# Optimization experiments

Measured on AMD Instinct MI355X. Metric: run time of the kernel, lower is better.

## Reference

```python
import jax, jax.numpy as jnp
from jax import lax
import numpy as np


def gen_position(p, pos_decay=1.0):
    # Fixed relative-position bias: (9, p*p), neighbor order di*3+dj
    ar = jnp.arange(p, dtype=jnp.float32)
    right = jnp.broadcast_to(jnp.exp(-ar / (p / pos_decay))[None, :], (p, p))  # decays along width
    down = right.T                                                             # decays along height
    i, j = jnp.meshgrid(ar, ar, indexing='ij')
    br = jnp.exp(-(i + j) / (p / pos_decay))
    ones = jnp.ones((p, p), jnp.float32)
    merge = jnp.stack([
        jnp.rot90(br, 2), down[::-1, :], jnp.rot90(br, 1),
        right[:, ::-1], ones, right,
        jnp.rot90(br, 3), down, br,
    ], axis=0)
    return merge.reshape(9, -1)


def attention_conv(x, w_qkv, b_qkv, head_w, window_size, num_heads):
    b, c, h, w = x.shape
    p = window_size // 3
    pad_h = (p * (1 + h // p) - h) % p
    pad_w = (p * (1 + w // p) - w) % p
    xp = jnp.pad(x, ((0, 0), (0, 0), (p + pad_h, p), (p + pad_w, p)), mode='reflect')
    Hp, Wp = xp.shape[2], xp.shape[3]
    nH, nW = Hp // p - 2, Wp // p - 2  # == number of unfold windows (stride p, size 3p)
    # Non-overlapping p x p tiles; each window = 3x3 grid of adjacent tiles.
    tiles = xp.reshape(b, c, nH + 2, p, nW + 2, p).transpose(0, 2, 4, 1, 3, 5)  # [b,nH+2,nW+2,c,p,p]
    neigh = jnp.stack([tiles[:, di:di + nH, dj:dj + nW]
                       for di in range(3) for dj in range(3)], axis=3)  # [b,nH,nW,9,c,p,p]
    L = c * p * p
    pp = p * p
    xw = neigh.reshape(b * nH * nW, 9, L)
    qkv = xw @ w_qkv.T + b_qkv                                  # [N,9,nh*3*L]
    qkv = qkv.reshape(-1, 9, num_heads, 3, c, pp).transpose(0, 2, 4, 3, 1, 5)  # [N,nh,C,3,9,pp]
    q, k, v = qkv[:, :, :, 0], qkv[:, :, :, 1], qkv[:, :, :, 2]  # each [N,nh,C,9,pp]
    bias = gen_position(p)                                       # [9,pp]
    core_q = q[:, :, :, 4, :]                                    # center patch query [N,nh,C,pp]
    score = jnp.einsum('nhcp,nhckp->nhck', core_q, k * bias) / jnp.sqrt(jnp.float32(L))
    attn = jax.nn.softmax(score, axis=-1)                        # over 9 neighbors
    out = jnp.einsum('nhck,nhckp->nhcp', attn, v).reshape(-1, num_heads, L)
    out = jnp.einsum('h,nhd->nd', head_w[0], out)                # head mixing [N,L]
    out = out.reshape(b, nH, nW, c, p, p).transpose(0, 3, 1, 4, 2, 5).reshape(b, c, nH * p, nW * p)
    return out[:, :, pad_h:, pad_w:]


def setup_inputs() -> dict:
    key = jax.random.key(0)
    ks = jax.random.split(key, 8)
    B, C, H, W = 4, 3, 256, 256
    x = jax.random.uniform(ks[0], (B, C, H, W), dtype=jnp.float32)
    # conv3: window 3, p=1, heads 6, L=3 ; conv6: window 6, p=2, heads 4, L=12 ; conv9: window 9, p=3, heads 2, L=27
    w3_qkv = jax.random.normal(ks[1], (6 * 3 * 3, 3), jnp.float32) * 0.2
    b3_qkv = jnp.zeros((6 * 3 * 3,), jnp.float32)
    hw3 = jnp.full((1, 6), 1.0 / 6.0, jnp.float32)
    w6_qkv = jax.random.normal(ks[2], (4 * 3 * 12, 12), jnp.float32) * 0.1
    b6_qkv = jnp.zeros((4 * 3 * 12,), jnp.float32)
    hw6 = jnp.full((1, 4), 1.0 / 4.0, jnp.float32)
    w9_qkv = jax.random.normal(ks[3], (2 * 3 * 27, 27), jnp.float32) * 0.07
    b9_qkv = jnp.zeros((2 * 3 * 27,), jnp.float32)
    hw9 = jnp.full((1, 2), 1.0 / 2.0, jnp.float32)
    conv0_w = jax.random.normal(ks[4], (3, 9, 5, 5), jnp.float32) * 0.05
    conv0_b = jnp.zeros((3,), jnp.float32)
    return {"x": x, "w3_qkv": w3_qkv, "b3_qkv": b3_qkv, "hw3": hw3,
            "w6_qkv": w6_qkv, "b6_qkv": b6_qkv, "hw6": hw6,
            "w9_qkv": w9_qkv, "b9_qkv": b9_qkv, "hw9": hw9,
            "conv0_w": conv0_w, "conv0_b": conv0_b}


def reference(x, w3_qkv, b3_qkv, hw3, w6_qkv, b6_qkv, hw6,
              w9_qkv, b9_qkv, hw9, conv0_w, conv0_b):
    b, c, h, w = x.shape
    # global prior: softmax over size-1 dim (== ones), then global max pool
    gavg = jnp.mean((1.0 - x).reshape(b, c, -1), axis=-1, keepdims=True)       # [b,c,1]
    x_g = jax.nn.softmax(gavg, axis=-1)[..., None]                             # [b,c,1,1]
    x_g = jnp.max((x * x_g).reshape(b, 1, -1), axis=-1, keepdims=True)[..., None]  # [b,1,1,1]
    x3 = attention_conv(x,  w3_qkv, b3_qkv, hw3, 3, 6)
    x6 = attention_conv(x3, w6_qkv, b6_qkv, hw6, 6, 4)
    x9 = attention_conv(x6, w9_qkv, b9_qkv, hw9, 9, 2)
    cat = jnp.concatenate([x9, x6, x3], axis=1)                                # [b,9,h,w]
    x0 = jax.nn.relu(lax.conv_general_dilated(cat, conv0_w, (1, 1), ((2, 2), (2, 2)),
                                              dimension_numbers=('NCHW', 'OIHW', 'NCHW'))
                     + conv0_b[None, :, None, None])
    return jax.nn.relu(x * x0 + (x_g - x0))
```

## Files before the change

kernel.cpp:

```cpp
#include <hip/hip_runtime.h>
#include <math.h>

__device__ __forceinline__ int refl256(int t) {
    t = t < 0 ? -t : t;
    return t > 255 ? 510 - t : t;
}

__global__ __launch_bounds__(256)
void attn_p1v(const float* __restrict__ x, const float* __restrict__ w,
              const float* __restrict__ bq, const float* __restrict__ hw,
              float* __restrict__ out, float* __restrict__ pmax)
{
    int t = blockIdx.x * 256 + threadIdx.x;
    int xx = t & 255, yp = (t >> 8) & 127, bb = t >> 15;
    int y0 = yp * 2;
    const float* xb = x + bb * 196608;
    int rs[4], cs[3];
#pragma unroll
    for (int dr = 0; dr < 4; ++dr) rs[dr] = refl256(y0 + dr - 1) << 8;
#pragma unroll
    for (int dc = 0; dc < 3; ++dc) cs[dc] = refl256(xx + dc - 1);
    float xw[4][3][3];
#pragma unroll
    for (int dr = 0; dr < 4; ++dr)
#pragma unroll
        for (int dc = 0; dc < 3; ++dc)
#pragma unroll
            for (int c = 0; c < 3; ++c)
                xw[dr][dc][c] = xb[c * 65536 + rs[dr] + cs[dc]];

    {
        float bm = 0.f;
#pragma unroll
        for (int c = 0; c < 3; ++c)
            bm = fmaxf(bm, fmaxf(xw[1][1][c], xw[2][1][c]));
#pragma unroll
        for (int off = 32; off > 0; off >>= 1)
            bm = fmaxf(bm, __shfl_down(bm, off, 64));
        __shared__ float sm[4];
        int lane = threadIdx.x & 63, wid = threadIdx.x >> 6;
        if (lane == 0) sm[wid] = bm;
        __syncthreads();
        if (threadIdx.x == 0)
            pmax[blockIdx.x] = fmaxf(fmaxf(sm[0], sm[1]), fmaxf(sm[2], sm[3]));
    }

    float ov0[3] = {0.f, 0.f, 0.f}, ov1[3] = {0.f, 0.f, 0.f};
    const float scl = 0.57735026919f;
#pragma unroll 1
    for (int h = 0; h < 6; ++h) {
        float hwh = hw[h];
#pragma unroll
        for (int cc = 0; cc < 3; ++cc) {
            int oq = 9 * h + cc, ok = oq + 3, oV = oq + 6;
            float wq0 = w[oq * 3], wq1 = w[oq * 3 + 1], wq2 = w[oq * 3 + 2];
            float wk0 = w[ok * 3], wk1 = w[ok * 3 + 1], wk2 = w[ok * 3 + 2];
            float wv0 = w[oV * 3], wv1 = w[oV * 3 + 1], wv2 = w[oV * 3 + 2];
            float bk = bq[ok], bv = bq[oV];
            float kp[12], vp[12];
#pragma unroll
            for (int pos = 0; pos < 12; ++pos) {
                const float* xv = xw[pos / 3][pos % 3];
                kp[pos] = fmaf(xv[0], wk0, fmaf(xv[1], wk1, fmaf(xv[2], wk2, bk)));
                vp[pos] = fmaf(xv[0], wv0, fmaf(xv[1], wv1, fmaf(xv[2], wv2, bv)));
            }
            float q0 = fmaf(xw[1][1][0], wq0, fmaf(xw[1][1][1], wq1, fmaf(xw[1][1][2], wq2, bq[oq]))) * scl;
            float q1 = fmaf(xw[2][1][0], wq0, fmaf(xw[2][1][1], wq1, fmaf(xw[2][1][2], wq2, bq[oq]))) * scl;
            float se0 = 0.f, ac0 = 0.f, se1 = 0.f, ac1 = 0.f;
#pragma unroll
            for (int j = 0; j < 9; ++j) {
                float e0 = __expf(q0 * kp[j]);
                se0 += e0; ac0 = fmaf(e0, vp[j], ac0);
                float e1 = __expf(q1 * kp[3 + j]);
                se1 += e1; ac1 = fmaf(e1, vp[3 + j], ac1);
            }
            ov0[cc] = fmaf(hwh, ac0 / se0, ov0[cc]);
            ov1[cc] = fmaf(hwh, ac1 / se1, ov1[cc]);
        }
    }
    int pix = (y0 << 8) + xx;
    float* ob = out + bb * 196608;
#pragma unroll
    for (int cc = 0; cc < 3; ++cc) {
        ob[cc * 65536 + pix] = ov0[cc];
        ob[cc * 65536 + pix + 256] = ov1[cc];
    }
}

template<int P, int NH, int NWIN, int OFS, int GSU, int NCH>
__global__ __launch_bounds__(64 * NCH)
void proj2_pk(const float* __restrict__ x, const float* __restrict__ w,
              const float* __restrict__ bq, float* __restrict__ kv)
{
    constexpr int PP = P * P, L = 3 * PP, NO = NH * 9 * PP, NG = NO / GSU;
    constexpr int CPG = NG / NCH;
    constexpr int NT = NWIN + 2, T4 = 4 * NT * NT;
    constexpr int LR = (L & 1) ? L : L + 1;
    __shared__ float s_x[64 * LR];
    const int tid = threadIdx.y * 64 + threadIdx.x;
    const int t0 = blockIdx.x * 64;
    for (int idx = tid; idx < 64 * L; idx += 64 * NCH) {
        int lane = idx & 63, l = idx >> 6;
        int t = t0 + lane;
        if (t < T4) {
            int bb = t / (NT * NT), rr = t - bb * NT * NT;
            int ty = rr / NT, tx = rr - ty * NT;
            int c = l / PP, pos = l - c * PP;
            int i = pos / P, j = pos - i * P;
            int pr = refl256(ty * P + i - OFS);
            int pc = refl256(tx * P + j - OFS);
            s_x[lane * LR + l] = x[bb * 196608 + c * 65536 + (pr << 8) + pc];
        }
    }
    __syncthreads();
    const int t = t0 + threadIdx.x;
    if (t >= T4) return;
    const int chunk = __builtin_amdgcn_readfirstlane((int)threadIdx.y);
    float xw[L];
#pragma unroll
    for (int l = 0; l < L; ++l) xw[l] = s_x[threadIdx.x * LR + l];
    float4* dst = (float4*)kv + t + (size_t)chunk * CPG * T4;
#pragma unroll 1
    for (int g = 0; g < CPG; ++g) {
        int go = (chunk * CPG + g) * GSU;
        float acc[GSU];
#pragma unroll
        for (int e = 0; e < GSU; ++e) acc[e] = bq[go + e];
#pragma unroll
        for (int l = 0; l < L; ++l) {
            float xv = xw[l];
#pragma unroll
            for (int e = 0; e < GSU; ++e)
                acc[e] = fmaf(xv, w[(go + e) * L + l], acc[e]);
        }
        float4 o4;
        o4.x = acc[0];
        o4.y = acc[1];
        o4.z = acc[2];
        o4.w = (GSU == 4) ? acc[GSU - 1] : 0.f;
        dst[(size_t)g * T4] = o4;
    }
}

template<int P, int NH, int NWIN, int OFS, int GSU>
__global__ __launch_bounds__(256)
void attn2_pk(const float* __restrict__ kv, const float* __restrict__ hw,
              float* __restrict__ out)
{
    constexpr int PP = P * P, NT = NWIN + 2, T4 = 4 * NT * NT, PAD = OFS - P;
    constexpr int NGP = (PP + GSU - 1) / GSU;
    constexpr float SCL = (P == 2) ? 0.28867513459481287f : 0.19245008972987526f;
    __shared__ float s_bias[9 * PP];
    int tid = threadIdx.x;
    if (tid < 9 * PP) {
        int j = tid / PP, pos = tid - j * PP;
        int i = pos / P, jj = pos - i * P;
        int di = j / 3, dj = j - di * 3;
        float er = (di == 0) ? (float)(P - 1 - i) : (di == 2 ? (float)i : 0.f);
        float ec = (dj == 0) ? (float)(P - 1 - jj) : (dj == 2 ? (float)jj : 0.f);
        s_bias[tid] = __expf(-(er + ec) / (float)P);
    }
    __syncthreads();
    int wlin = blockIdx.x * 256 + tid;
    if (wlin >= 4 * NWIN * NWIN) return;
    int c = blockIdx.y;
    int bb = wlin / (NWIN * NWIN); int rr = wlin - bb * NWIN * NWIN;
    int yy = rr / NWIN, xx = rr - yy * NWIN;
    int tbase = bb * NT * NT + yy * NT + xx;
    int tn[9];
#pragma unroll
    for (int di = 0; di < 3; ++di)
#pragma unroll
        for (int dj = 0; dj < 3; ++dj) tn[di * 3 + dj] = tbase + di * NT + dj;
    const float4* kv4 = (const float4*)kv;
    float oa[PP];
#pragma unroll
    for (int e = 0; e < PP; ++e) oa[e] = 0.f;
#pragma unroll 1
    for (int h = 0; h < NH; ++h) {
        int oq = ((h * 3 + 0) * 3 + c) * PP;
        int ok = ((h * 3 + 1) * 3 + c) * PP;
        int ov = ((h * 3 + 2) * 3 + c) * PP;
        int gq = oq / GSU, gk = ok / GSU, gv = ov / GSU;
        float q[PP];
#pragma unroll
        for (int u = 0; u < NGP; ++u) {
            float4 t4 = kv4[(size_t)(gq + u) * T4 + tn[4]];
            float g4[4] = {t4.x, t4.y, t4.z, t4.w};
#pragma unroll
            for (int e = 0; e < GSU; ++e) q[u * GSU + e] = g4[e];
        }
        float sc[9];
#pragma unroll
        for (int j = 0; j < 9; ++j) {
            float s = 0.f;
#pragma unroll
            for (int u = 0; u < NGP; ++u) {
                float4 t4 = kv4[(size_t)(gk + u) * T4 + tn[j]];
                float g4[4] = {t4.x, t4.y, t4.z, t4.w};
#pragma unroll
                for (int e = 0; e < GSU; ++e) {
                    int Pp = u * GSU + e;
                    s = fmaf(q[Pp] * g4[e], s_bias[j * PP + Pp], s);
                }
            }
            sc[j] = s * SCL;
        }
        float se = 0.f;
#pragma unroll
        for (int j = 0; j < 9; ++j) { sc[j] = __expf(sc[j]); se += sc[j]; }
        float tmp[PP];
#pragma unroll
        for (int e = 0; e < PP; ++e) tmp[e] = 0.f;
#pragma unroll
        for (int j = 0; j < 9; ++j) {
#pragma unroll
            for (int u = 0; u < NGP; ++u) {
                float4 t4 = kv4[(size_t)(gv + u) * T4 + tn[j]];
                float g4[4] = {t4.x, t4.y, t4.z, t4.w};
#pragma unroll
                for (int e = 0; e < GSU; ++e)
                    tmp[u * GSU + e] = fmaf(sc[j], g4[e], tmp[u * GSU + e]);
            }
        }
        float f = hw[h] / se;
#pragma unroll
        for (int e = 0; e < PP; ++e) oa[e] = fmaf(f, tmp[e], oa[e]);
    }
    float* ob = out + (bb * 3 + c) * 65536;
#pragma unroll
    for (int i = 0; i < P; ++i) {
        int r = yy * P + i - PAD;
        if (PAD && r < 0) continue;
#pragma unroll
        for (int jj = 0; jj < P; ++jj) {
            int col = xx * P + jj - PAD;
            if (PAD && col < 0) continue;
            ob[(r << 8) + col] = oa[i * P + jj];
        }
    }
}

__global__ __launch_bounds__(256)
void conv_finalv(const float* __restrict__ x, const float* __restrict__ x9,
                 const float* __restrict__ x6, const float* __restrict__ x3,
                 const float* __restrict__ cw, const float* __restrict__ cb,
                 const float* __restrict__ pmax, float* __restrict__ out)
{
    int tid = threadIdx.x;
    int bb = blockIdx.x >> 6;
    __shared__ float red[128];
    __shared__ float s_g;
    if (tid < 128) red[tid] = pmax[bb * 128 + tid];
    __syncthreads();
    if (tid < 64) {
        float v = fmaxf(red[tid], red[tid + 64]);
#pragma unroll
        for (int off = 32; off > 0; off >>= 1)
            v = fmaxf(v, __shfl_down(v, off, 64));
        if (tid == 0) s_g = v;
    }
    __syncthreads();

    int gid = blockIdx.x * 256 + tid;
    int xq = (gid & 63) << 2, r = (gid >> 6) & 255;
    float a[3][4];
#pragma unroll
    for (int oc = 0; oc < 3; ++oc) {
        float b = cb[oc];
#pragma unroll
        for (int p = 0; p < 4; ++p) a[oc][p] = b;
    }
#pragma unroll 1
    for (int s = 0; s < 3; ++s) {
        const float* bp = (s == 0 ? x9 : (s == 1 ? x6 : x3)) + bb * 196608;
#pragma unroll 1
        for (int c2 = 0; c2 < 3; ++c2) {
            const float* pl = bp + c2 * 65536;
            const float* wp = cw + (s * 3 + c2) * 25;
#pragma unroll
            for (int ky = 0; ky < 5; ++ky) {
                int rr = r + ky - 2;
                if ((unsigned)rr >= 256u) continue;
                const float* row = pl + (rr << 8);
                float cv[8];
                cv[0] = (xq >= 2) ? row[xq - 2] : 0.f;
                cv[1] = (xq >= 1) ? row[xq - 1] : 0.f;
                float4 m4 = *(const float4*)(row + xq);
                cv[2] = m4.x; cv[3] = m4.y; cv[4] = m4.z; cv[5] = m4.w;
                cv[6] = (xq + 4 < 256) ? row[xq + 4] : 0.f;
                cv[7] = (xq + 5 < 256) ? row[xq + 5] : 0.f;
#pragma unroll
                for (int kx = 0; kx < 5; ++kx) {
                    float w0 = wp[ky * 5 + kx];
                    float w1 = wp[225 + ky * 5 + kx];
                    float w2 = wp[450 + ky * 5 + kx];
#pragma unroll
                    for (int p = 0; p < 4; ++p) {
                        float v = cv[kx + p];
                        a[0][p] = fmaf(v, w0, a[0][p]);
                        a[1][p] = fmaf(v, w1, a[1][p]);
                        a[2][p] = fmaf(v, w2, a[2][p]);
                    }
                }
            }
        }
    }
    float g = s_g;
    int pix = (r << 8) + xq;
    const float* xb = x + bb * 196608;
    float* ob = out + bb * 196608;
#pragma unroll
    for (int oc = 0; oc < 3; ++oc) {
        float4 xv = *(const float4*)(xb + oc * 65536 + pix);
        float4 o4;
        float x0;
        x0 = fmaxf(a[oc][0], 0.f); o4.x = fmaxf(xv.x * x0 + g - x0, 0.f);
        x0 = fmaxf(a[oc][1], 0.f); o4.y = fmaxf(xv.y * x0 + g - x0, 0.f);
        x0 = fmaxf(a[oc][2], 0.f); o4.z = fmaxf(xv.z * x0 + g - x0, 0.f);
        x0 = fmaxf(a[oc][3], 0.f); o4.w = fmaxf(xv.w * x0 + g - x0, 0.f);
        *(float4*)(ob + oc * 65536 + pix) = o4;
    }
}

extern "C" void kernel_launch(void* const* d_in, const int* in_sizes, int n_in,
                              void* d_out, int out_size, void* d_ws, size_t ws_size,
                              hipStream_t stream)
{
    const float* x   = (const float*)d_in[0];
    const float* w3  = (const float*)d_in[1];
    const float* b3  = (const float*)d_in[2];
    const float* hw3 = (const float*)d_in[3];
    const float* w6  = (const float*)d_in[4];
    const float* b6  = (const float*)d_in[5];
    const float* hw6 = (const float*)d_in[6];
    const float* w9  = (const float*)d_in[7];
    const float* b9  = (const float*)d_in[8];
    const float* hw9 = (const float*)d_in[9];
    const float* cw  = (const float*)d_in[10];
    const float* cb  = (const float*)d_in[11];

    float* ws   = (float*)d_ws;
    float* x3b  = ws;
    float* x6b  = ws + 786432;
    float* x9b  = ws + 1572864;
    float* pmax = ws + 2359296;
    float* kvb  = ws + 2359808;
    float* out  = (float*)d_out;

    attn_p1v<<<512, 256, 0, stream>>>(x, w3, b3, hw3, x3b, pmax);

    proj2_pk<2, 4, 128, 2, 4, 6><<<1057, dim3(64, 6), 0, stream>>>(x3b, w6, b6, kvb);
    attn2_pk<2, 4, 128, 2, 4><<<dim3(256, 3), 256, 0, stream>>>(kvb, hw6, x6b);
    proj2_pk<3, 2, 86, 5, 3, 9><<<484, dim3(64, 9), 0, stream>>>(x6b, w9, b9, kvb);
    attn2_pk<3, 2, 86, 5, 3><<<dim3(116, 3), 256, 0, stream>>>(kvb, hw9, x9b);

    conv_finalv<<<256, 256, 0, stream>>>(x, x9b, x6b, x3b, cw, cb, pmax, out);
}
```

Before: 178.2 us.

## Fuse QKV projection and neighborhood attention into one tiled kernel per stage

Replaces the separate projection kernel (which wrote q/k/v to a global buffer) and attention kernel with a single kernel per stage. Each block loads a tile of windows plus a one-tile halo into shared memory, computes q/k/v for all tiles into LDS, then runs the 9-neighbor softmax attention from LDS. This removes the global round trip for the large kv buffer and two launches. In exchange, halo tiles are projected redundantly by neighbouring blocks, the shared-memory footprint is large enough to limit occupancy, and only 3*WB*WB threads are active in the attention phase.

```diff
diff --git a/kernel.cpp b/kernel.cpp
--- a/kernel.cpp
+++ b/kernel.cpp
@@ -87,71 +87,30 @@
     }
 }
 
-template<int P, int NH, int NWIN, int OFS, int GSU, int NCH>
-__global__ __launch_bounds__(64 * NCH)
-void proj2_pk(const float* __restrict__ x, const float* __restrict__ w,
-              const float* __restrict__ bq, float* __restrict__ kv)
+template<int P, int NH, int WB, int OFS, int NBLK, int NWIN>
+__global__ __launch_bounds__(192)
+void fused_attn(const float* __restrict__ x, const float* __restrict__ w,
+                const float* __restrict__ bq, const float* __restrict__ hw,
+                float* __restrict__ out)
 {
-    constexpr int PP = P * P, L = 3 * PP, NO = NH * 9 * PP, NG = NO / GSU;
-    constexpr int CPG = NG / NCH;
-    constexpr int NT = NWIN + 2, T4 = 4 * NT * NT;
-    constexpr int LR = (L & 1) ? L : L + 1;
-    __shared__ float s_x[64 * LR];
-    const int tid = threadIdx.y * 64 + threadIdx.x;
-    const int t0 = blockIdx.x * 64;
-    for (int idx = tid; idx < 64 * L; idx += 64 * NCH) {
-        int lane = idx & 63, l = idx >> 6;
-        int t = t0 + lane;
-        if (t < T4) {
-            int bb = t / (NT * NT), rr = t - bb * NT * NT;
-            int ty = rr / NT, tx = rr - ty * NT;
-            int c = l / PP, pos = l - c * PP;
-            int i = pos / P, j = pos - i * P;
-            int pr = refl256(ty * P + i - OFS);
-            int pc = refl256(tx * P + j - OFS);
-            s_x[lane * LR + l] = x[bb * 196608 + c * 65536 + (pr << 8) + pc];
-        }
-    }
-    __syncthreads();
-    const int t = t0 + threadIdx.x;
-    if (t >= T4) return;
-    const int chunk = __builtin_amdgcn_readfirstlane((int)threadIdx.y);
-    float xw[L];
-#pragma unroll
-    for (int l = 0; l < L; ++l) xw[l] = s_x[threadIdx.x * LR + l];
-    float4* dst = (float4*)kv + t + (size_t)chunk * CPG * T4;
-#pragma unroll 1
-    for (int g = 0; g < CPG; ++g) {
-        int go = (chunk * CPG + g) * GSU;
-        float acc[GSU];
-#pragma unroll
-        for (int e = 0; e < GSU; ++e) acc[e] = bq[go + e];
-#pragma unroll
-        for (int l = 0; l < L; ++l) {
-            float xv = xw[l];
-#pragma unroll
-            for (int e = 0; e < GSU; ++e)
-                acc[e] = fmaf(xv, w[(go + e) * L + l], acc[e]);
-        }
-        float4 o4;
-        o4.x = acc[0];
-        o4.y = acc[1];
-        o4.z = acc[2];
-        o4.w = (GSU == 4) ? acc[GSU - 1] : 0.f;
-        dst[(size_t)g * T4] = o4;
-    }
-}
-
-template<int P, int NH, int NWIN, int OFS, int GSU>
-__global__ __launch_bounds__(256)
-void attn2_pk(const float* __restrict__ kv, const float* __restrict__ hw,
-              float* __restrict__ out)
-{
-    constexpr int PP = P * P, NT = NWIN + 2, T4 = 4 * NT * NT, PAD = OFS - P;
-    constexpr int NGP = (PP + GSU - 1) / GSU;
+    constexpr int PP = P * P, L = 3 * PP, NO = NH * 9 * PP;
+    constexpr int TB = WB + 2, TT = TB * TB;
+    constexpr int LP = L | 1;
+    constexpr int PAD = OFS - P;
+    constexpr int OPW = NO / 3;
     constexpr float SCL = (P == 2) ? 0.28867513459481287f : 0.19245008972987526f;
+
+    __shared__ float s_x[TT * LP];
+    __shared__ float s_kv[NO * TT];
     __shared__ float s_bias[9 * PP];
-    int tid = threadIdx.x;
+
+    const int tid = threadIdx.x;
+    int blk = blockIdx.x;
+    int bb = blk / (NBLK * NBLK);
+    int r2 = blk - bb * (NBLK * NBLK);
+    int by = r2 / NBLK, bx = r2 - by * NBLK;
+    const int wy0 = by * WB, wx0 = bx * WB;
+
     if (tid < 9 * PP) {
         int j = tid / PP, pos = tid - j * PP;
         int i = pos / P, jj = pos - i * P;
@@ -160,83 +119,94 @@
         float ec = (dj == 0) ? (float)(P - 1 - jj) : (dj == 2 ? (float)jj : 0.f);
         s_bias[tid] = __expf(-(er + ec) / (float)P);
     }
+
+    const float* xb = x + bb * 196608;
+    for (int idx = tid; idx < TT * L; idx += 192) {
+        int t = idx / L, l = idx - t * L;
+        int trow = t / TB, tcol = t - trow * TB;
+        int c = l / PP, pos = l - c * PP;
+        int i = pos / P, j = pos - i * P;
+        int pr = refl256((wy0 + trow) * P + i - OFS);
+        int pc = refl256((wx0 + tcol) * P + j - OFS);
+        s_x[t * LP + l] = xb[c * 65536 + (pr << 8) + pc];
+    }
     __syncthreads();
-    int wlin = blockIdx.x * 256 + tid;
-    if (wlin >= 4 * NWIN * NWIN) return;
-    int c = blockIdx.y;
-    int bb = wlin / (NWIN * NWIN); int rr = wlin - bb * NWIN * NWIN;
-    int yy = rr / NWIN, xx = rr - yy * NWIN;
-    int tbase = bb * NT * NT + yy * NT + xx;
-    int tn[9];
-#pragma unroll
-    for (int di = 0; di < 3; ++di)
-#pragma unroll
-        for (int dj = 0; dj < 3; ++dj) tn[di * 3 + dj] = tbase + di * NT + dj;
-    const float4* kv4 = (const float4*)kv;
-    float oa[PP];
-#pragma unroll
-    for (int e = 0; e < PP; ++e) oa[e] = 0.f;
-#pragma unroll 1
-    for (int h = 0; h < NH; ++h) {
-        int oq = ((h * 3 + 0) * 3 + c) * PP;
-        int ok = ((h * 3 + 1) * 3 + c) * PP;
-        int ov = ((h * 3 + 2) * 3 + c) * PP;
-        int gq = oq / GSU, gk = ok / GSU, gv = ov / GSU;
-        float q[PP];
-#pragma unroll
-        for (int u = 0; u < NGP; ++u) {
-            float4 t4 = kv4[(size_t)(gq + u) * T4 + tn[4]];
-            float g4[4] = {t4.x, t4.y, t4.z, t4.w};
-#pragma unroll
-            for (int e = 0; e < GSU; ++e) q[u * GSU + e] = g4[e];
+
+    {
+        const int wave = __builtin_amdgcn_readfirstlane(tid >> 6);
+        const int lane = tid & 63;
+#pragma unroll 1
+        for (int c0 = 0; c0 < TT; c0 += 64) {
+            int t = c0 + lane;
+            bool tv = t < TT;
+            int ts = tv ? t : 0;
+            float xw[L];
+#pragma unroll
+            for (int l = 0; l < L; ++l) xw[l] = s_x[ts * LP + l];
+#pragma unroll 4
+            for (int oi = 0; oi < OPW; ++oi) {
+                int o = wave * OPW + oi;
+                float acc = bq[o];
+                const float* wr = w + o * L;
+#pragma unroll
+                for (int l = 0; l < L; ++l) acc = fmaf(xw[l], wr[l], acc);
+                if (tv) s_kv[o * TT + t] = acc;
+            }
         }
-        float sc[9];
-#pragma unroll
-        for (int j = 0; j < 9; ++j) {
-            float s = 0.f;
-#pragma unroll
-            for (int u = 0; u < NGP; ++u) {
-                float4 t4 = kv4[(size_t)(gk + u) * T4 + tn[j]];
-                float g4[4] = {t4.x, t4.y, t4.z, t4.w};
-#pragma unroll
-                for (int e = 0; e < GSU; ++e) {
-                    int Pp = u * GSU + e;
-                    s = fmaf(q[Pp] * g4[e], s_bias[j * PP + Pp], s);
+    }
+    __syncthreads();
+
+    if (tid < 3 * WB * WB) {
+        int c = tid / (WB * WB), wl = tid - c * (WB * WB);
+        int wy = wl / WB, wx = wl - wy * WB;
+        int gy = wy0 + wy, gx = wx0 + wx;
+        if (gy < NWIN && gx < NWIN) {
+            int tc = (wy + 1) * TB + (wx + 1);
+            float oa[PP];
+#pragma unroll
+            for (int e = 0; e < PP; ++e) oa[e] = 0.f;
+#pragma unroll 1
+            for (int h = 0; h < NH; ++h) {
+                int bqo = ((h * 3 + 0) * 3 + c) * PP;
+                int bko = ((h * 3 + 1) * 3 + c) * PP;
+                int bvo = ((h * 3 + 2) * 3 + c) * PP;
+                float q[PP];
+#pragma unroll
+                for (int e = 0; e < PP; ++e)
+                    q[e] = s_kv[(bqo + e) * TT + tc] * SCL;
+                float se = 0.f;
+                float tmp[PP];
+#pragma unroll
+                for (int e = 0; e < PP; ++e) tmp[e] = 0.f;
+#pragma unroll
+                for (int j = 0; j < 9; ++j) {
+                    int tj = (wy + j / 3) * TB + (wx + j % 3);
+                    float s = 0.f;
+#pragma unroll
+                    for (int e = 0; e < PP; ++e)
+                        s = fmaf(q[e] * s_kv[(bko + e) * TT + tj], s_bias[j * PP + e], s);
+                    float ex = __expf(s);
+                    se += ex;
+#pragma unroll
+                    for (int e = 0; e < PP; ++e)
+                        tmp[e] = fmaf(ex, s_kv[(bvo + e) * TT + tj], tmp[e]);
                 }
-            }
-            sc[j] = s * SCL;
-        }
-        float se = 0.f;
-#pragma unroll
-        for (int j = 0; j < 9; ++j) { sc[j] = __expf(sc[j]); se += sc[j]; }
-        float tmp[PP];
-#pragma unroll
-        for (int e = 0; e < PP; ++e) tmp[e] = 0.f;
-#pragma unroll
-        for (int j = 0; j < 9; ++j) {
-#pragma unroll
-            for (int u = 0; u < NGP; ++u) {
-                float4 t4 = kv4[(size_t)(gv + u) * T4 + tn[j]];
-                float g4[4] = {t4.x, t4.y, t4.z, t4.w};
-#pragma unroll
-                for (int e = 0; e < GSU; ++e)
-                    tmp[u * GSU + e] = fmaf(sc[j], g4[e], tmp[u * GSU + e]);
-            }
-        }
-        float f = hw[h] / se;
-#pragma unroll
-        for (int e = 0; e < PP; ++e) oa[e] = fmaf(f, tmp[e], oa[e]);
-    }
-    float* ob = out + (bb * 3 + c) * 65536;
-#pragma unroll
-    for (int i = 0; i < P; ++i) {
-        int r = yy * P + i - PAD;
-        if (PAD && r < 0) continue;
-#pragma unroll
-        for (int jj = 0; jj < P; ++jj) {
-            int col = xx * P + jj - PAD;
-            if (PAD && col < 0) continue;
-            ob[(r << 8) + col] = oa[i * P + jj];
+                float f = hw[h] / se;
+#pragma unroll
+                for (int e = 0; e < PP; ++e) oa[e] = fmaf(f, tmp[e], oa[e]);
+            }
+            float* ob = out + (bb * 3 + c) * 65536;
+#pragma unroll
+            for (int i = 0; i < P; ++i) {
+                int r = gy * P + i - PAD;
+                if (PAD && r < 0) continue;
+#pragma unroll
+                for (int jj = 0; jj < P; ++jj) {
+                    int col = gx * P + jj - PAD;
+                    if (PAD && col < 0) continue;
+                    ob[(r << 8) + col] = oa[i * P + jj];
+                }
+            }
         }
     }
 }
@@ -345,15 +315,12 @@
     float* x6b  = ws + 786432;
     float* x9b  = ws + 1572864;
     float* pmax = ws + 2359296;
-    float* kvb  = ws + 2359808;
     float* out  = (float*)d_out;
 
     attn_p1v<<<512, 256, 0, stream>>>(x, w3, b3, hw3, x3b, pmax);
 
-    proj2_pk<2, 4, 128, 2, 4, 6><<<1057, dim3(64, 6), 0, stream>>>(x3b, w6, b6, kvb);
-    attn2_pk<2, 4, 128, 2, 4><<<dim3(256, 3), 256, 0, stream>>>(kvb, hw6, x6b);
-    proj2_pk<3, 2, 86, 5, 3, 9><<<484, dim3(64, 9), 0, stream>>>(x6b, w9, b9, kvb);
-    attn2_pk<3, 2, 86, 5, 3><<<dim3(116, 3), 256, 0, stream>>>(kvb, hw9, x9b);
+    fused_attn<2, 4, 8, 2, 16, 128><<<1024, 192, 0, stream>>>(x3b, w6, b6, hw6, x6b);
+    fused_attn<3, 2, 7, 5, 13, 86><<<676, 192, 0, stream>>>(x6b, w9, b9, hw9, x9b);
 
     conv_finalv<<<256, 256, 0, stream>>>(x, x9b, x6b, x3b, cw, cb, pmax, out);
 }
```

Measured after the change: 217.6 us. 1.22x slower.
